# Optimization experiments

Hardware: AMD Instinct MI355X
Metric: run time of the kernel (lower is better)

The kernel has to match this reference:

```python
import jax, jax.numpy as jnp
import numpy as np

E = 8          # moe_expert_count
CAPACITY = 1024  # per-expert capacity C = S / E (capacity factor 1)


def _top1_gate(features, wg):
    """Top-1 gate with capacity, returning combine_weights [S,E,C],
    dispatch_mask [S,E,C], and load-balancing aux loss (standard Switch/BASE-style gate
    matching the (l_aux, combine_weights, dispatch_mask) interface used by BaseLayer)."""
    S, M = features.shape
    logits = features @ wg                      # [S, E]
    gates = jax.nn.softmax(logits, axis=-1)     # [S, E]
    idx = jnp.argmax(gates, axis=-1)            # [S] expert assignment
    mask1 = jax.nn.one_hot(idx, E, dtype=features.dtype)  # [S, E]
    # position of each token inside its expert's buffer (0-based, order of arrival)
    locations = jnp.cumsum(mask1, axis=0) - mask1          # [S, E]
    loc = jnp.sum(locations * mask1, axis=1).astype(jnp.int32)  # [S]
    keep = (loc < CAPACITY).astype(features.dtype)          # drop overflow tokens
    mask1 = mask1 * keep[:, None]
    gate_s = jnp.sum(gates * mask1, axis=1)                 # [S] gate prob of kept tokens
    loc_oh = jax.nn.one_hot(loc, CAPACITY, dtype=features.dtype)  # [S, C]
    combine = gate_s[:, None, None] * mask1[:, :, None] * loc_oh[:, None, :]  # [S,E,C]
    dispatch = (combine > 0).astype(features.dtype)
    # load-balance aux loss: E * sum(mean_prob_e * frac_tokens_e)
    me = jnp.mean(gates, axis=0)
    ce = jnp.mean(mask1, axis=0)
    l_aux = jnp.sum(me * ce) * E
    return l_aux, combine, dispatch


def setup_inputs() -> dict:
    key = jax.random.key(0)
    k0, k1, k2, k3 = jax.random.split(key, 4)
    B, T, M, H = 4, 2048, 512, 1024
    return {
        "hidden_states": jax.random.normal(k0, (B, T, M), dtype=jnp.float32),
        "wg": jax.random.normal(k1, (M, E), dtype=jnp.float32) * 0.02,
        "w1": jax.random.normal(k2, (E, M, H), dtype=jnp.float32) * 0.02,
        "b1": jnp.zeros((E, H), dtype=jnp.float32),
        "w2": jax.random.normal(k3, (E, H, M), dtype=jnp.float32) * 0.02,
        "b2": jnp.zeros((E, M), dtype=jnp.float32),
    }


def reference(hidden_states, wg, w1, b1, w2, b2):
    B, T, M = hidden_states.shape
    feats = hidden_states.reshape(-1, M)            # [S, M]
    l_aux, combine, dispatch = _top1_gate(feats, wg)
    # dense one-hot dispatch matmul: (E*C, S) @ (S, M) -> [E, C, M]
    dispatched = jnp.einsum('sec,sm->ecm', dispatch, feats)
    # per-expert FFN (BaseSublayer: Linear -> ReLU -> Linear)
    h = jax.nn.relu(jnp.einsum('ecm,emh->ech', dispatched, w1) + b1[:, None, :])
    expert_out = jnp.einsum('ech,ehn->ecn', h, w2) + b2[:, None, :]  # [E, C, M]
    # dense combine matmul: (S, E*C) @ (E*C, M) -> [S, M]
    combined = jnp.einsum('sec,ecn->sn', combine, expert_out)
    return combined.reshape(B, T, -1), l_aux
```

## Files before the change

kernel.cpp:

```cpp
#include <hip/hip_runtime.h>

#define S_TOK 8192
#define M_DIM 512
#define E_NUM 8
#define CAP   1024
#define H_DIM 1024
#define NGATE_BLK (S_TOK / 4)

typedef __attribute__((ext_vector_type(8))) short bf16x8;
typedef __attribute__((ext_vector_type(4))) float f32x4;

__device__ static inline unsigned short f2bf(float f) {
    unsigned int u = __float_as_uint(f);
    unsigned int r = (u + 0x7fffu + ((u >> 16) & 1u)) >> 16;
    return (unsigned short)r;
}

__device__ static inline void async_copy16(const void* g, void* l) {
    __builtin_amdgcn_global_load_lds(
        (const __attribute__((address_space(1))) void*)g,
        (__attribute__((address_space(3))) void*)l, 16, 0, 0);
}

__global__ __launch_bounds__(256) void prep_kernel(
    const float* __restrict__ feats, const float* __restrict__ wg,
    int* __restrict__ idx, float* __restrict__ gate_top,
    float* __restrict__ gates_psum, unsigned short* __restrict__ xb,
    const float* __restrict__ w1, unsigned short* __restrict__ w1t,
    const float* __restrict__ w2, unsigned short* __restrict__ w2t)
{
    __shared__ float gsh[4][8];
    __shared__ float tile[64][65];

    if (blockIdx.x < NGATE_BLK) {
        const int wave = threadIdx.x >> 6;
        const int lane = threadIdx.x & 63;
        const int s = blockIdx.x * 4 + wave;

        const float* xrow = feats + (size_t)s * M_DIM;
        const int m0 = lane * 8;

        const float4 va = *(const float4*)(xrow + m0);
        const float4 vb = *(const float4*)(xrow + m0 + 4);
        float xv[8] = {va.x, va.y, va.z, va.w, vb.x, vb.y, vb.z, vb.w};

        {
            bf16x8 o;
#pragma unroll
            for (int j = 0; j < 8; ++j) o[j] = (short)f2bf(xv[j]);
            *(bf16x8*)(xb + (size_t)s * M_DIM + m0) = o;
            if (blockIdx.x == 0 && wave == 0) {
                bf16x8 z = (bf16x8){0,0,0,0,0,0,0,0};
                *(bf16x8*)(xb + (size_t)S_TOK * M_DIM + m0) = z;
            }
        }

        float p[8];
#pragma unroll
        for (int e = 0; e < 8; ++e) p[e] = 0.f;
#pragma unroll
        for (int j = 0; j < 8; ++j) {
            const float4 wa = *(const float4*)(wg + (m0 + j) * 8);
            const float4 wb2 = *(const float4*)(wg + (m0 + j) * 8 + 4);
            const float x = xv[j];
            p[0] += x * wa.x;  p[1] += x * wa.y;  p[2] += x * wa.z;  p[3] += x * wa.w;
            p[4] += x * wb2.x; p[5] += x * wb2.y; p[6] += x * wb2.z; p[7] += x * wb2.w;
        }
#pragma unroll
        for (int e = 0; e < 8; ++e) {
            float v = p[e];
#pragma unroll
            for (int off = 1; off < 64; off <<= 1) v += __shfl_xor(v, off, 64);
            p[e] = v;
        }
        if (lane == 0) {
            float mx = p[0];
#pragma unroll
            for (int e = 1; e < 8; ++e) mx = fmaxf(mx, p[e]);
            float ex[8], sum = 0.f;
#pragma unroll
            for (int e = 0; e < 8; ++e) { ex[e] = expf(p[e] - mx); sum += ex[e]; }
            const float inv = 1.0f / sum;
            int best = 0; float bl = p[0];
#pragma unroll
            for (int e = 1; e < 8; ++e) { if (p[e] > bl) { bl = p[e]; best = e; } }
#pragma unroll
            for (int e = 0; e < 8; ++e) gsh[wave][e] = ex[e] * inv;
            idx[s] = best;
            gate_top[s] = ex[best] * inv;
        }
        __syncthreads();
        if (threadIdx.x < 8) {
            const int e = threadIdx.x;
            gates_psum[blockIdx.x * 8 + e] =
                gsh[0][e] + gsh[1][e] + gsh[2][e] + gsh[3][e];
        }
    } else {
        int b = blockIdx.x - NGATE_BLK;
        const float* src; unsigned short* dst;
        int e, k0, n0, K, N;
        if (b < 1024) {
            e = b >> 7; const int rem = b & 127;
            k0 = (rem >> 4) * 64; n0 = (rem & 15) * 64;
            K = 512; N = 1024; src = w1; dst = w1t;
        } else {
            b -= 1024;
            e = b >> 7; const int rem = b & 127;
            k0 = (rem >> 3) * 64; n0 = (rem & 7) * 64;
            K = 1024; N = 512; src = w2; dst = w2t;
        }
        const int t = threadIdx.x;
        const int r = t >> 4, c4 = (t & 15) * 4;
#pragma unroll
        for (int i = 0; i < 4; ++i) {
            const int row = r + i * 16;
            const float4 v = *(const float4*)(src + ((size_t)e * K + k0 + row) * N + n0 + c4);
            tile[row][c4 + 0] = v.x; tile[row][c4 + 1] = v.y;
            tile[row][c4 + 2] = v.z; tile[row][c4 + 3] = v.w;
        }
        __syncthreads();
#pragma unroll
        for (int i = 0; i < 4; ++i) {
            const int row = r + i * 16;
            ushort4 o;
            o.x = f2bf(tile[c4 + 0][row]); o.y = f2bf(tile[c4 + 1][row]);
            o.z = f2bf(tile[c4 + 2][row]); o.w = f2bf(tile[c4 + 3][row]);
            *(ushort4*)(dst + ((size_t)e * N + n0 + row) * K + k0 + c4) = o;
        }
    }
}

__global__ __launch_bounds__(256) void scan_kernel(
    const int* __restrict__ idx, const float* __restrict__ gate_top,
    const float* __restrict__ gates_psum,
    float* __restrict__ gate_final, int* __restrict__ token_list,
    int* __restrict__ kept, float* __restrict__ out)
{
    __shared__ int   cnts[256][9];
    __shared__ float wpart[4][8];
    __shared__ int   totals[8];
    __shared__ int   sdrop[7168];
    __shared__ int   dropctr;

    const int t = threadIdx.x;
    const int wv = t >> 6, ln = t & 63;
    const int base = t * 32;

    for (int i = t; i < E_NUM * CAP; i += 256) token_list[i] = S_TOK;
    if (t == 0) dropctr = 0;

    int c[8];
#pragma unroll
    for (int e = 0; e < 8; ++e) c[e] = 0;
    for (int i = 0; i < 32; ++i) {
        const int ei = idx[base + i];
#pragma unroll
        for (int e = 0; e < 8; ++e) c[e] += (ei == e) ? 1 : 0;
    }
    float g[8];
#pragma unroll
    for (int e = 0; e < 8; ++e) g[e] = 0.f;
    for (int i = 0; i < NGATE_BLK / 256; ++i) {
        const float* gp = gates_psum + (size_t)(t + 256 * i) * 8;
        const float4 a = *(const float4*)gp;
        const float4 b = *(const float4*)(gp + 4);
        g[0] += a.x; g[1] += a.y; g[2] += a.z; g[3] += a.w;
        g[4] += b.x; g[5] += b.y; g[6] += b.z; g[7] += b.w;
    }
#pragma unroll
    for (int e = 0; e < 8; ++e) cnts[t][e] = c[e];
#pragma unroll
    for (int e = 0; e < 8; ++e) {
        float v = g[e];
#pragma unroll
        for (int off = 1; off < 64; off <<= 1) v += __shfl_xor(v, off, 64);
        if (ln == 0) wpart[wv][e] = v;
    }
    __syncthreads();

#pragma unroll
    for (int ee = 0; ee < 2; ++ee) {
        const int e = wv * 2 + ee;
        int off = 0;
#pragma unroll
        for (int seg = 0; seg < 4; ++seg) {
            const int r = seg * 64 + ln;
            const int v = cnts[r][e];
            int incl = v;
#pragma unroll
            for (int d = 1; d < 64; d <<= 1) {
                const int nn = __shfl_up(incl, d, 64);
                if (ln >= d) incl += nn;
            }
            cnts[r][e] = incl - v + off;
            off += __shfl(incl, 63, 64);
        }
        if (ln == 0) {
            totals[e] = off;
            kept[e] = off < CAP ? off : CAP;
        }
    }
    __syncthreads();

    if (t == 0) {
        float l = 0.f;
        for (int e = 0; e < 8; ++e) {
            const float ms = wpart[0][e] + wpart[1][e] + wpart[2][e] + wpart[3][e];
            const int ke = totals[e] < CAP ? totals[e] : CAP;
            l += (ms / (float)S_TOK) * ((float)ke / (float)S_TOK);
        }
        out[(size_t)S_TOK * M_DIM] = l * (float)E_NUM;
    }

    int rc[8];
#pragma unroll
    for (int e = 0; e < 8; ++e) rc[e] = cnts[t][e];

    for (int i = 0; i < 32; ++i) {
        const int s = base + i;
        const int ei = idx[s];
        int loc = 0;
#pragma unroll
        for (int e = 0; e < 8; ++e) {
            if (ei == e) { loc = rc[e]; rc[e] = rc[e] + 1; }
        }
        const bool keepit = loc < CAP;
        gate_final[s] = keepit ? gate_top[s] : 0.f;
        if (keepit) {
            token_list[ei * CAP + loc] = s;
        } else {
            const int d = atomicAdd(&dropctr, 1);
            sdrop[d] = s;
        }
    }
    __syncthreads();

    const int nd = dropctr;
    for (int d = wv; d < nd; d += 4) {
        const int s = sdrop[d];
        float4 z = make_float4(0.f, 0.f, 0.f, 0.f);
        *(float4*)(out + (size_t)s * M_DIM + ln * 4) = z;
        *(float4*)(out + (size_t)s * M_DIM + 256 + ln * 4) = z;
    }
}

__global__ __launch_bounds__(256, 3) void ffn1_mfma(
    const unsigned short* __restrict__ xb, const unsigned short* __restrict__ w1t,
    const float* __restrict__ b1, const int* __restrict__ tok,
    const int* __restrict__ kept, unsigned short* __restrict__ h)
{
    const int b = blockIdx.x;
    const int e = b & 7;
    const int r = b >> 3;
    const int ct = r >> 4, nt = r & 15;
    const int c0 = ct * 128, n0 = nt * 64;
    if (c0 >= kept[e]) return;

    __shared__ __align__(16) short Alds[2][128 * 64];
    __shared__ __align__(16) short Blds[2][64 * 64];
    __shared__ int srow[128];

    const int t = threadIdx.x;
    const int wave = t >> 6, lane = t & 63;
    const int wm = wave & 1, wn = wave >> 1;
    const int q = lane >> 4, lr = lane & 15;

    if (t < 128) srow[t] = tok[e * CAP + c0 + t];
    __syncthreads();

    auto stage = [&](int buf, int kb) {
#pragma unroll
        for (int i = 0; i < 4; ++i) {
            const int lin = (i * 4 + wave) * 64 + lane;
            const int row = lin >> 3;
            const int ch = (lin & 7) ^ (row & 7);
            async_copy16(xb + (size_t)srow[row] * M_DIM + kb + ch * 8,
                         &Alds[buf][lin * 8]);
        }
#pragma unroll
        for (int i = 0; i < 2; ++i) {
            const int lin = (i * 4 + wave) * 64 + lane;
            const int row = lin >> 3;
            const int ch = (lin & 7) ^ (row & 7);
            async_copy16(w1t + ((size_t)e * H_DIM + n0 + row) * M_DIM + kb + ch * 8,
                         &Blds[buf][lin * 8]);
        }
    };

    f32x4 acc[4][2];
#pragma unroll
    for (int mi = 0; mi < 4; ++mi)
#pragma unroll
        for (int ni = 0; ni < 2; ++ni) acc[mi][ni] = (f32x4){0.f, 0.f, 0.f, 0.f};

    stage(0, 0);

    int cur = 0;
    for (int kb = 0; kb < M_DIM; kb += 64) {
        __syncthreads();
        if (kb + 64 < M_DIM) stage(cur ^ 1, kb + 64);

#pragma unroll
        for (int kk = 0; kk < 64; kk += 32) {
            const int cb = kk >> 3;
            bf16x8 af[4], bfv[2];
#pragma unroll
            for (int mi = 0; mi < 4; ++mi) {
                const int R = wm * 64 + mi * 16 + lr;
                af[mi] = *(const bf16x8*)(&Alds[cur][(R * 8 + ((cb + q) ^ (R & 7))) * 8]);
            }
#pragma unroll
            for (int ni = 0; ni < 2; ++ni) {
                const int R = wn * 32 + ni * 16 + lr;
                bfv[ni] = *(const bf16x8*)(&Blds[cur][(R * 8 + ((cb + q) ^ (R & 7))) * 8]);
            }
#pragma unroll
            for (int mi = 0; mi < 4; ++mi)
#pragma unroll
                for (int ni = 0; ni < 2; ++ni)
                    acc[mi][ni] = __builtin_amdgcn_mfma_f32_16x16x32_bf16(
                        af[mi], bfv[ni], acc[mi][ni], 0, 0, 0);
        }
        cur ^= 1;
    }

#pragma unroll
    for (int ni = 0; ni < 2; ++ni) {
        const int col = n0 + wn * 32 + ni * 16 + lr;
        const float bias = b1[e * H_DIM + col];
#pragma unroll
        for (int mi = 0; mi < 4; ++mi) {
            const int rowl = wm * 64 + mi * 16 + q * 4;
            const size_t basep = (size_t)(e * CAP + c0 + rowl) * H_DIM + col;
#pragma unroll
            for (int r2 = 0; r2 < 4; ++r2) {
                const float v = fmaxf(acc[mi][ni][r2] + bias, 0.f);
                h[basep + (size_t)r2 * H_DIM] = f2bf(v);
            }
        }
    }
}

__global__ __launch_bounds__(256, 4) void ffn2_mfma(
    const unsigned short* __restrict__ h, const unsigned short* __restrict__ w2t,
    const float* __restrict__ b2, const int* __restrict__ tok,
    const int* __restrict__ kept, const float* __restrict__ gate_final,
    float* __restrict__ out)
{
    const int b = blockIdx.x;
    const int e = b & 7;
    const int r = b >> 3;
    const int ct = r >> 3, nt = r & 7;
    const int c0 = ct * 64, n0 = nt * 64;
    if (c0 >= kept[e]) return;

    __shared__ __align__(16) short Alds[2][64 * 64];
    __shared__ __align__(16) short Blds[2][64 * 64];
    __shared__ int   stok[64];
    __shared__ float sgf[64];

    const int t = threadIdx.x;
    const int wave = t >> 6, lane = t & 63;
    const int wm = wave & 1, wn = wave >> 1;
    const int q = lane >> 4, lr = lane & 15;

    if (t < 64) {
        const int tk = tok[e * CAP + c0 + t];
        stok[t] = tk;
        sgf[t] = (tk != S_TOK) ? gate_final[tk] : 0.f;
    }

    auto stage = [&](int buf, int kb) {
#pragma unroll
        for (int i = 0; i < 2; ++i) {
            const int lin = (i * 4 + wave) * 64 + lane;
            const int row = lin >> 3;
            const int ch = (lin & 7) ^ (row & 7);
            async_copy16(h + (size_t)(e * CAP + c0 + row) * H_DIM + kb + ch * 8,
                         &Alds[buf][lin * 8]);
        }
#pragma unroll
        for (int i = 0; i < 2; ++i) {
            const int lin = (i * 4 + wave) * 64 + lane;
            const int row = lin >> 3;
            const int ch = (lin & 7) ^ (row & 7);
            async_copy16(w2t + ((size_t)e * M_DIM + n0 + row) * H_DIM + kb + ch * 8,
                         &Blds[buf][lin * 8]);
        }
    };

    f32x4 acc[2][2];
#pragma unroll
    for (int mi = 0; mi < 2; ++mi)
#pragma unroll
        for (int ni = 0; ni < 2; ++ni) acc[mi][ni] = (f32x4){0.f, 0.f, 0.f, 0.f};

    stage(0, 0);

    int cur = 0;
    for (int kb = 0; kb < H_DIM; kb += 64) {
        __syncthreads();
        if (kb + 64 < H_DIM) stage(cur ^ 1, kb + 64);

#pragma unroll
        for (int kk = 0; kk < 64; kk += 32) {
            const int cb = kk >> 3;
            bf16x8 af[2], bfv[2];
#pragma unroll
            for (int mi = 0; mi < 2; ++mi) {
                const int R = wm * 32 + mi * 16 + lr;
                af[mi] = *(const bf16x8*)(&Alds[cur][(R * 8 + ((cb + q) ^ (R & 7))) * 8]);
            }
#pragma unroll
            for (int ni = 0; ni < 2; ++ni) {
                const int R = wn * 32 + ni * 16 + lr;
                bfv[ni] = *(const bf16x8*)(&Blds[cur][(R * 8 + ((cb + q) ^ (R & 7))) * 8]);
            }
#pragma unroll
            for (int mi = 0; mi < 2; ++mi)
#pragma unroll
                for (int ni = 0; ni < 2; ++ni)
                    acc[mi][ni] = __builtin_amdgcn_mfma_f32_16x16x32_bf16(
                        af[mi], bfv[ni], acc[mi][ni], 0, 0, 0);
        }
        cur ^= 1;
    }

#pragma unroll
    for (int ni = 0; ni < 2; ++ni) {
        const int col = n0 + wn * 32 + ni * 16 + lr;
        const float bias = b2[e * M_DIM + col];
#pragma unroll
        for (int mi = 0; mi < 2; ++mi) {
            const int rowl = wm * 32 + mi * 16 + q * 4;
#pragma unroll
            for (int r2 = 0; r2 < 4; ++r2) {
                const int slot = rowl + r2;
                const int tokid = stok[slot];
                if (tokid != S_TOK) {
                    out[(size_t)tokid * M_DIM + col] = sgf[slot] * (acc[mi][ni][r2] + bias);
                }
            }
        }
    }
}

extern "C" void kernel_launch(void* const* d_in, const int* in_sizes, int n_in,
                              void* d_out, int out_size, void* d_ws, size_t ws_size,
                              hipStream_t stream) {
    const float* feats = (const float*)d_in[0];
    const float* wg    = (const float*)d_in[1];
    const float* w1    = (const float*)d_in[2];
    const float* b1    = (const float*)d_in[3];
    const float* w2    = (const float*)d_in[4];
    const float* b2    = (const float*)d_in[5];
    float* out = (float*)d_out;

    char* ws = (char*)d_ws;
    size_t off = 0;
    unsigned short* h   = (unsigned short*)(ws + off); off += (size_t)E_NUM * CAP * H_DIM * 2;
    unsigned short* xb  = (unsigned short*)(ws + off); off += (size_t)(S_TOK + 1) * M_DIM * 2;
    unsigned short* w1t = (unsigned short*)(ws + off); off += (size_t)E_NUM * H_DIM * M_DIM * 2;
    unsigned short* w2t = (unsigned short*)(ws + off); off += (size_t)E_NUM * M_DIM * H_DIM * 2;
    int*   idx        = (int*)(ws + off);   off += (size_t)S_TOK * 4;
    float* gate_top   = (float*)(ws + off); off += (size_t)S_TOK * 4;
    float* gate_final = (float*)(ws + off); off += (size_t)S_TOK * 4;
    float* gates_psum = (float*)(ws + off); off += (size_t)NGATE_BLK * 8 * 4;
    int*   token_list = (int*)(ws + off);   off += (size_t)S_TOK * 4;
    int*   kept       = (int*)(ws + off);   off += 64;
    (void)ws_size; (void)n_in; (void)in_sizes;

    prep_kernel<<<NGATE_BLK + 2048, 256, 0, stream>>>(
        feats, wg, idx, gate_top, gates_psum, xb, w1, w1t, w2, w2t);
    scan_kernel<<<1, 256, 0, stream>>>(idx, gate_top, gates_psum, gate_final,
                                       token_list, kept, out);
    ffn1_mfma<<<1024, 256, 0, stream>>>(xb, w1t, b1, token_list, kept, h);
    ffn2_mfma<<<1024, 256, 0, stream>>>(h, w2t, b2, token_list, kept,
                                        gate_final, out);
}
```

Measured before the change: 182.9 us.

## Switch FFN GEMMs to 32x32x16 MFMA and drop LDS double buffering

Both expert FFN kernels now use the 32x32x16 bf16 MFMA instruction with 16-float accumulators instead of tiles of 16x16x32 MFMAs. The LDS staging goes from double-buffered prefetch to a single buffer with a barrier after each load. ffn1 launch bounds rise to 4 blocks per CU. The goal is fewer LDS fragment reads per MFMA and more occupancy from the halved LDS use, at the cost of losing load/compute overlap inside each block.

```diff
diff --git a/kernel.cpp b/kernel.cpp
--- a/kernel.cpp
+++ b/kernel.cpp
@@ -8,7 +8,7 @@
 #define NGATE_BLK (S_TOK / 4)
 
 typedef __attribute__((ext_vector_type(8))) short bf16x8;
-typedef __attribute__((ext_vector_type(4))) float f32x4;
+typedef __attribute__((ext_vector_type(16))) float f32x16;
 
 __device__ static inline unsigned short f2bf(float f) {
     unsigned int u = __float_as_uint(f);
@@ -244,7 +244,7 @@
     }
 }
 
-__global__ __launch_bounds__(256, 3) void ffn1_mfma(
+__global__ __launch_bounds__(256, 4) void ffn1_mfma(
     const unsigned short* __restrict__ xb, const unsigned short* __restrict__ w1t,
     const float* __restrict__ b1, const int* __restrict__ tok,
     const int* __restrict__ kept, unsigned short* __restrict__ h)
@@ -256,26 +256,33 @@
     const int c0 = ct * 128, n0 = nt * 64;
     if (c0 >= kept[e]) return;
 
-    __shared__ __align__(16) short Alds[2][128 * 64];
-    __shared__ __align__(16) short Blds[2][64 * 64];
+    __shared__ __align__(16) short Alds[128 * 64];
+    __shared__ __align__(16) short Blds[64 * 64];
     __shared__ int srow[128];
 
     const int t = threadIdx.x;
     const int wave = t >> 6, lane = t & 63;
     const int wm = wave & 1, wn = wave >> 1;
-    const int q = lane >> 4, lr = lane & 15;
+    const int l31 = lane & 31, kh = lane >> 5;
 
     if (t < 128) srow[t] = tok[e * CAP + c0 + t];
     __syncthreads();
 
-    auto stage = [&](int buf, int kb) {
+    f32x16 acc[2];
+#pragma unroll
+    for (int mg = 0; mg < 2; ++mg)
+#pragma unroll
+        for (int i = 0; i < 16; ++i) acc[mg][i] = 0.f;
+
+    for (int kb = 0; kb < M_DIM; kb += 64) {
+        __syncthreads();
 #pragma unroll
         for (int i = 0; i < 4; ++i) {
             const int lin = (i * 4 + wave) * 64 + lane;
             const int row = lin >> 3;
             const int ch = (lin & 7) ^ (row & 7);
             async_copy16(xb + (size_t)srow[row] * M_DIM + kb + ch * 8,
-                         &Alds[buf][lin * 8]);
+                         &Alds[lin * 8]);
         }
 #pragma unroll
         for (int i = 0; i < 2; ++i) {
@@ -283,60 +290,39 @@
             const int row = lin >> 3;
             const int ch = (lin & 7) ^ (row & 7);
             async_copy16(w1t + ((size_t)e * H_DIM + n0 + row) * M_DIM + kb + ch * 8,
-                         &Blds[buf][lin * 8]);
-        }
-    };
-
-    f32x4 acc[4][2];
-#pragma unroll
-    for (int mi = 0; mi < 4; ++mi)
-#pragma unroll
-        for (int ni = 0; ni < 2; ++ni) acc[mi][ni] = (f32x4){0.f, 0.f, 0.f, 0.f};
-
-    stage(0, 0);
-
-    int cur = 0;
-    for (int kb = 0; kb < M_DIM; kb += 64) {
-        __syncthreads();
-        if (kb + 64 < M_DIM) stage(cur ^ 1, kb + 64);
-
-#pragma unroll
-        for (int kk = 0; kk < 64; kk += 32) {
-            const int cb = kk >> 3;
-            bf16x8 af[4], bfv[2];
-#pragma unroll
-            for (int mi = 0; mi < 4; ++mi) {
-                const int R = wm * 64 + mi * 16 + lr;
-                af[mi] = *(const bf16x8*)(&Alds[cur][(R * 8 + ((cb + q) ^ (R & 7))) * 8]);
-            }
-#pragma unroll
-            for (int ni = 0; ni < 2; ++ni) {
-                const int R = wn * 32 + ni * 16 + lr;
-                bfv[ni] = *(const bf16x8*)(&Blds[cur][(R * 8 + ((cb + q) ^ (R & 7))) * 8]);
-            }
-#pragma unroll
-            for (int mi = 0; mi < 4; ++mi)
-#pragma unroll
-                for (int ni = 0; ni < 2; ++ni)
-                    acc[mi][ni] = __builtin_amdgcn_mfma_f32_16x16x32_bf16(
-                        af[mi], bfv[ni], acc[mi][ni], 0, 0, 0);
-        }
-        cur ^= 1;
-    }
-
-#pragma unroll
-    for (int ni = 0; ni < 2; ++ni) {
-        const int col = n0 + wn * 32 + ni * 16 + lr;
-        const float bias = b1[e * H_DIM + col];
-#pragma unroll
-        for (int mi = 0; mi < 4; ++mi) {
-            const int rowl = wm * 64 + mi * 16 + q * 4;
-            const size_t basep = (size_t)(e * CAP + c0 + rowl) * H_DIM + col;
-#pragma unroll
-            for (int r2 = 0; r2 < 4; ++r2) {
-                const float v = fmaxf(acc[mi][ni][r2] + bias, 0.f);
-                h[basep + (size_t)r2 * H_DIM] = f2bf(v);
-            }
+                         &Blds[lin * 8]);
+        }
+        __syncthreads();
+
+#pragma unroll
+        for (int kk = 0; kk < 64; kk += 16) {
+            const int ch = (kk >> 3) + kh;
+            bf16x8 af[2], bfv;
+#pragma unroll
+            for (int mg = 0; mg < 2; ++mg) {
+                const int R = wm * 64 + mg * 32 + l31;
+                af[mg] = *(const bf16x8*)(&Alds[(R * 8 + (ch ^ (R & 7))) * 8]);
+            }
+            {
+                const int R = wn * 32 + l31;
+                bfv = *(const bf16x8*)(&Blds[(R * 8 + (ch ^ (R & 7))) * 8]);
+            }
+#pragma unroll
+            for (int mg = 0; mg < 2; ++mg)
+                acc[mg] = __builtin_amdgcn_mfma_f32_32x32x16_bf16(
+                    af[mg], bfv, acc[mg], 0, 0, 0);
+        }
+    }
+
+    const int col = n0 + wn * 32 + l31;
+    const float bias = b1[e * H_DIM + col];
+#pragma unroll
+    for (int mg = 0; mg < 2; ++mg) {
+#pragma unroll
+        for (int reg = 0; reg < 16; ++reg) {
+            const int rowl = wm * 64 + mg * 32 + (reg & 3) + 8 * (reg >> 2) + 4 * kh;
+            const float v = fmaxf(acc[mg][reg] + bias, 0.f);
+            h[(size_t)(e * CAP + c0 + rowl) * H_DIM + col] = f2bf(v);
         }
     }
 }
@@ -354,15 +340,15 @@
     const int c0 = ct * 64, n0 = nt * 64;
     if (c0 >= kept[e]) return;
 
-    __shared__ __align__(16) short Alds[2][64 * 64];
-    __shared__ __align__(16) short Blds[2][64 * 64];
+    __shared__ __align__(16) short Alds[64 * 64];
+    __shared__ __align__(16) short Blds[64 * 64];
     __shared__ int   stok[64];
     __shared__ float sgf[64];
 
     const int t = threadIdx.x;
     const int wave = t >> 6, lane = t & 63;
     const int wm = wave & 1, wn = wave >> 1;
-    const int q = lane >> 4, lr = lane & 15;
+    const int l31 = lane & 31, kh = lane >> 5;
 
     if (t < 64) {
         const int tk = tok[e * CAP + c0 + t];
@@ -370,14 +356,19 @@
         sgf[t] = (tk != S_TOK) ? gate_final[tk] : 0.f;
     }
 
-    auto stage = [&](int buf, int kb) {
+    f32x16 acc;
+#pragma unroll
+    for (int i = 0; i < 16; ++i) acc[i] = 0.f;
+
+    for (int kb = 0; kb < H_DIM; kb += 64) {
+        __syncthreads();
 #pragma unroll
         for (int i = 0; i < 2; ++i) {
             const int lin = (i * 4 + wave) * 64 + lane;
             const int row = lin >> 3;
             const int ch = (lin & 7) ^ (row & 7);
             async_copy16(h + (size_t)(e * CAP + c0 + row) * H_DIM + kb + ch * 8,
-                         &Alds[buf][lin * 8]);
+                         &Alds[lin * 8]);
         }
 #pragma unroll
         for (int i = 0; i < 2; ++i) {
@@ -385,62 +376,34 @@
             const int row = lin >> 3;
             const int ch = (lin & 7) ^ (row & 7);
             async_copy16(w2t + ((size_t)e * M_DIM + n0 + row) * H_DIM + kb + ch * 8,
-                         &Blds[buf][lin * 8]);
-        }
-    };
-
-    f32x4 acc[2][2];
-#pragma unroll
-    for (int mi = 0; mi < 2; ++mi)
-#pragma unroll
-        for (int ni = 0; ni < 2; ++ni) acc[mi][ni] = (f32x4){0.f, 0.f, 0.f, 0.f};
-
-    stage(0, 0);
-
-    int cur = 0;
-    for (int kb = 0; kb < H_DIM; kb += 64) {
-        __syncthreads();
-        if (kb + 64 < H_DIM) stage(cur ^ 1, kb + 64);
-
-#pragma unroll
-        for (int kk = 0; kk < 64; kk += 32) {
-            const int cb = kk >> 3;
-            bf16x8 af[2], bfv[2];
-#pragma unroll
-            for (int mi = 0; mi < 2; ++mi) {
-                const int R = wm * 32 + mi * 16 + lr;
-                af[mi] = *(const bf16x8*)(&Alds[cur][(R * 8 + ((cb + q) ^ (R & 7))) * 8]);
-            }
-#pragma unroll
-            for (int ni = 0; ni < 2; ++ni) {
-                const int R = wn * 32 + ni * 16 + lr;
-                bfv[ni] = *(const bf16x8*)(&Blds[cur][(R * 8 + ((cb + q) ^ (R & 7))) * 8]);
-            }
-#pragma unroll
-            for (int mi = 0; mi < 2; ++mi)
-#pragma unroll
-                for (int ni = 0; ni < 2; ++ni)
-                    acc[mi][ni] = __builtin_amdgcn_mfma_f32_16x16x32_bf16(
-                        af[mi], bfv[ni], acc[mi][ni], 0, 0, 0);
-        }
-        cur ^= 1;
-    }
-
-#pragma unroll
-    for (int ni = 0; ni < 2; ++ni) {
-        const int col = n0 + wn * 32 + ni * 16 + lr;
-        const float bias = b2[e * M_DIM + col];
-#pragma unroll
-        for (int mi = 0; mi < 2; ++mi) {
-            const int rowl = wm * 32 + mi * 16 + q * 4;
-#pragma unroll
-            for (int r2 = 0; r2 < 4; ++r2) {
-                const int slot = rowl + r2;
-                const int tokid = stok[slot];
-                if (tokid != S_TOK) {
-                    out[(size_t)tokid * M_DIM + col] = sgf[slot] * (acc[mi][ni][r2] + bias);
-                }
-            }
+                         &Blds[lin * 8]);
+        }
+        __syncthreads();
+
+#pragma unroll
+        for (int kk = 0; kk < 64; kk += 16) {
+            const int ch = (kk >> 3) + kh;
+            bf16x8 af, bfv;
+            {
+                const int R = wm * 32 + l31;
+                af = *(const bf16x8*)(&Alds[(R * 8 + (ch ^ (R & 7))) * 8]);
+            }
+            {
+                const int R = wn * 32 + l31;
+                bfv = *(const bf16x8*)(&Blds[(R * 8 + (ch ^ (R & 7))) * 8]);
+            }
+            acc = __builtin_amdgcn_mfma_f32_32x32x16_bf16(af, bfv, acc, 0, 0, 0);
+        }
+    }
+
+    const int col = n0 + wn * 32 + l31;
+    const float bias = b2[e * M_DIM + col];
+#pragma unroll
+    for (int reg = 0; reg < 16; ++reg) {
+        const int slot = wm * 32 + (reg & 3) + 8 * (reg >> 2) + 4 * kh;
+        const int tokid = stok[slot];
+        if (tokid != S_TOK) {
+            out[(size_t)tokid * M_DIM + col] = sgf[slot] * (acc[reg] + bias);
         }
     }
 }
```

Result: faster. 177.4 us (-3.0%).
